# Kernel optimization log

Measured on AMD Instinct MI355X. Metric: run time of the kernel, lower is better.

The kernel has to match this reference:

```python
import jax, jax.numpy as jnp
import numpy as np

EMBED = 1024
B, I, J = 8, 2048, 2048
SCALE = EMBED ** -0.5


def setup_inputs() -> dict:
    key = jax.random.key(0)
    ks = jax.random.split(key, 5)
    s = EMBED ** -0.5  # init scale for weights
    return {
        "q_in": jax.random.normal(ks[0], (B, I, EMBED), dtype=jnp.float32),
        "k_v": jax.random.normal(ks[1], (B, J, EMBED), dtype=jnp.float32),
        "Wq": jax.random.normal(ks[2], (EMBED, EMBED), dtype=jnp.float32) * s,
        "bq": jnp.zeros((EMBED,), dtype=jnp.float32),
        "Wk": jax.random.normal(ks[3], (EMBED, EMBED), dtype=jnp.float32) * s,
        "bk": jnp.zeros((EMBED,), dtype=jnp.float32),
        "Wv": jax.random.normal(ks[4], (EMBED, EMBED), dtype=jnp.float32) * s,
        "bv": jnp.zeros((EMBED,), dtype=jnp.float32),
    }


def reference(q_in, k_v, Wq, bq, Wk, bk, Wv, bv):
    # Linear projections (torch Linear: x @ W.T + b; here W stored as [in, out])
    q = q_in @ Wq + bq            # [b, i, d]
    k = k_v @ Wk + bk             # [b, j, d]
    v = k_v @ Wv + bv             # [b, j, d]
    sim = jnp.einsum('bid,bjd->bij', q, k) * SCALE  # [b, i, j]
    attn = jax.nn.softmax(sim, axis=-1)
    # dropout with drop_rate=0.0 is identity
    out = jnp.einsum('bij,bjd->bid', attn, v)       # [b, i, d]
    return out
```

## Files before the change

kernel.cpp:

```cpp
#include <hip/hip_runtime.h>
#include <hip/hip_bf16.h>


#define BATCH 8
#define SEQ   2048
#define EMB   1024
#define SC2   0.045084222f

typedef __attribute__((ext_vector_type(8))) short bf16x8;
typedef __attribute__((ext_vector_type(4))) float f32x4;
typedef __attribute__((ext_vector_type(4))) unsigned short u16x4;
typedef __attribute__((ext_vector_type(8))) unsigned short u16x8;
typedef __attribute__((ext_vector_type(4))) unsigned int u32x4;
typedef __attribute__((ext_vector_type(4))) float fl4;

__device__ __forceinline__ unsigned short f2bf(float f) {
    unsigned u = __builtin_bit_cast(unsigned, f);
    unsigned r = u + 0x7fffu + ((u >> 16) & 1u);
    return (unsigned short)(r >> 16);
}
__device__ __forceinline__ float bf2f(unsigned short s) {
    return __builtin_bit_cast(float, ((unsigned)s) << 16);
}
__device__ __forceinline__ unsigned cvtpk(float a, float b) {
    unsigned r;
    asm("v_cvt_pk_bf16_f32 %0, %1, %2" : "=v"(r) : "v"(a), "v"(b));
    return r;
}
__device__ __forceinline__ void gload16(const unsigned short* g, unsigned short* l) {
    __builtin_amdgcn_global_load_lds(
        (const __attribute__((address_space(1))) void*)g,
        (__attribute__((address_space(3))) void*)l, 16, 0, 0);
}

__global__ __launch_bounds__(256)
void convert_w(const float* __restrict__ Wq, const float* __restrict__ Wk,
               const float* __restrict__ Wv, unsigned short* __restrict__ Wt)
{
    const int wsel = blockIdx.y;
    const float* W = (wsel == 0) ? Wq : (wsel == 1) ? Wk : Wv;
    unsigned short* O = Wt + (size_t)wsel * EMB * EMB;
    const int k0 = (blockIdx.x >> 4) * 64;
    const int n0 = (blockIdx.x & 15) * 64;
    __shared__ unsigned short l[64 * 65];
    const int tid = threadIdx.x;
#pragma unroll
    for (int it = 0; it < 16; it++) {
        const int lin = it * 256 + tid;
        const int k = lin >> 6, n = lin & 63;
        l[n * 65 + k] = f2bf(W[(size_t)(k0 + k) * EMB + n0 + n]);
    }
    __syncthreads();
#pragma unroll
    for (int it = 0; it < 16; it++) {
        const int lin = it * 256 + tid;
        const int n = lin >> 6, k = lin & 63;
        O[(size_t)(n0 + n) * EMB + k0 + k] = l[n * 65 + k];
    }
}

__device__ __forceinline__ void stageT(const unsigned short* lanebase, size_t rstride,
                                       unsigned short* lwave) {
#pragma unroll
    for (int i = 0; i < 2; i++)
        gload16(lanebase + (size_t)(i * 128) * rstride, lwave + i * 4096);
}

#define MFMA16_LO(A0,A1,A2,A3)                                                  \
        acc[0][0] = __builtin_amdgcn_mfma_f32_16x16x32_bf16(A0, bv0, acc[0][0], 0, 0, 0); \
        acc[0][1] = __builtin_amdgcn_mfma_f32_16x16x32_bf16(A0, bv1, acc[0][1], 0, 0, 0); \
        acc[0][2] = __builtin_amdgcn_mfma_f32_16x16x32_bf16(A0, bv2, acc[0][2], 0, 0, 0); \
        acc[0][3] = __builtin_amdgcn_mfma_f32_16x16x32_bf16(A0, bv3, acc[0][3], 0, 0, 0); \
        acc[1][0] = __builtin_amdgcn_mfma_f32_16x16x32_bf16(A1, bv0, acc[1][0], 0, 0, 0); \
        acc[1][1] = __builtin_amdgcn_mfma_f32_16x16x32_bf16(A1, bv1, acc[1][1], 0, 0, 0); \
        acc[1][2] = __builtin_amdgcn_mfma_f32_16x16x32_bf16(A1, bv2, acc[1][2], 0, 0, 0); \
        acc[1][3] = __builtin_amdgcn_mfma_f32_16x16x32_bf16(A1, bv3, acc[1][3], 0, 0, 0); \
        acc[2][0] = __builtin_amdgcn_mfma_f32_16x16x32_bf16(A2, bv0, acc[2][0], 0, 0, 0); \
        acc[2][1] = __builtin_amdgcn_mfma_f32_16x16x32_bf16(A2, bv1, acc[2][1], 0, 0, 0); \
        acc[2][2] = __builtin_amdgcn_mfma_f32_16x16x32_bf16(A2, bv2, acc[2][2], 0, 0, 0); \
        acc[2][3] = __builtin_amdgcn_mfma_f32_16x16x32_bf16(A2, bv3, acc[2][3], 0, 0, 0); \
        acc[3][0] = __builtin_amdgcn_mfma_f32_16x16x32_bf16(A3, bv0, acc[3][0], 0, 0, 0); \
        acc[3][1] = __builtin_amdgcn_mfma_f32_16x16x32_bf16(A3, bv1, acc[3][1], 0, 0, 0); \
        acc[3][2] = __builtin_amdgcn_mfma_f32_16x16x32_bf16(A3, bv2, acc[3][2], 0, 0, 0); \
        acc[3][3] = __builtin_amdgcn_mfma_f32_16x16x32_bf16(A3, bv3, acc[3][3], 0, 0, 0);

#define MFMA16_HI(A4,A5,A6,A7)                                                  \
        acc[4][0] = __builtin_amdgcn_mfma_f32_16x16x32_bf16(A4, bv0, acc[4][0], 0, 0, 0); \
        acc[4][1] = __builtin_amdgcn_mfma_f32_16x16x32_bf16(A4, bv1, acc[4][1], 0, 0, 0); \
        acc[4][2] = __builtin_amdgcn_mfma_f32_16x16x32_bf16(A4, bv2, acc[4][2], 0, 0, 0); \
        acc[4][3] = __builtin_amdgcn_mfma_f32_16x16x32_bf16(A4, bv3, acc[4][3], 0, 0, 0); \
        acc[5][0] = __builtin_amdgcn_mfma_f32_16x16x32_bf16(A5, bv0, acc[5][0], 0, 0, 0); \
        acc[5][1] = __builtin_amdgcn_mfma_f32_16x16x32_bf16(A5, bv1, acc[5][1], 0, 0, 0); \
        acc[5][2] = __builtin_amdgcn_mfma_f32_16x16x32_bf16(A5, bv2, acc[5][2], 0, 0, 0); \
        acc[5][3] = __builtin_amdgcn_mfma_f32_16x16x32_bf16(A5, bv3, acc[5][3], 0, 0, 0); \
        acc[6][0] = __builtin_amdgcn_mfma_f32_16x16x32_bf16(A6, bv0, acc[6][0], 0, 0, 0); \
        acc[6][1] = __builtin_amdgcn_mfma_f32_16x16x32_bf16(A6, bv1, acc[6][1], 0, 0, 0); \
        acc[6][2] = __builtin_amdgcn_mfma_f32_16x16x32_bf16(A6, bv2, acc[6][2], 0, 0, 0); \
        acc[6][3] = __builtin_amdgcn_mfma_f32_16x16x32_bf16(A6, bv3, acc[6][3], 0, 0, 0); \
        acc[7][0] = __builtin_amdgcn_mfma_f32_16x16x32_bf16(A7, bv0, acc[7][0], 0, 0, 0); \
        acc[7][1] = __builtin_amdgcn_mfma_f32_16x16x32_bf16(A7, bv1, acc[7][1], 0, 0, 0); \
        acc[7][2] = __builtin_amdgcn_mfma_f32_16x16x32_bf16(A7, bv2, acc[7][2], 0, 0, 0); \
        acc[7][3] = __builtin_amdgcn_mfma_f32_16x16x32_bf16(A7, bv3, acc[7][3], 0, 0, 0);

#define FRAG_READS(SLOT)                                                        \
        const unsigned short* pa = &sA[SLOT][0];                                \
        const unsigned short* pb = &sB[SLOT][0];                                \
        bf16x8 a0 = *(bf16x8*)&pa[aoff0];                                       \
        bf16x8 a1 = *(bf16x8*)&pa[aoff0 + 512];                                 \
        bf16x8 a2 = *(bf16x8*)&pa[aoff0 + 1024];                                \
        bf16x8 a3 = *(bf16x8*)&pa[aoff0 + 1536];                                \
        bf16x8 a4 = *(bf16x8*)&pa[aoff0 + 2048];                                \
        bf16x8 a5 = *(bf16x8*)&pa[aoff0 + 2560];                                \
        bf16x8 a6 = *(bf16x8*)&pa[aoff0 + 3072];                                \
        bf16x8 a7 = *(bf16x8*)&pa[aoff0 + 3584];                                \
        bf16x8 bv0 = *(bf16x8*)&pb[boff0];                                      \
        bf16x8 bv1 = *(bf16x8*)&pb[boff0 + 512];                                \
        bf16x8 bv2 = *(bf16x8*)&pb[boff0 + 1024];                               \
        bf16x8 bv3 = *(bf16x8*)&pb[boff0 + 1536];

__device__ __forceinline__ void pipe_gemm(
    const unsigned short* __restrict__ Asrc,
    const unsigned short* __restrict__ Bsrc,
    const size_t strideA, const size_t strideB, const int NT,
    unsigned short (*sA)[8192], unsigned short (*sB)[8192],
    const int lwave, const int aoff0, const int boff0,
    f32x4 acc[8][4])
{
    stageT(Asrc, strideA, &sA[0][lwave]);
    stageT(Bsrc, strideB, &sB[0][lwave]);
    stageT(Asrc + 32, strideA, &sA[1][lwave]);
    stageT(Bsrc + 32, strideB, &sB[1][lwave]);
    asm volatile("s_waitcnt vmcnt(4)" ::: "memory");
    __builtin_amdgcn_s_barrier();
    __builtin_amdgcn_sched_barrier(0);

    for (int T = 0; T < NT; ++T) {
        const int s = T & 3;
        const int doStage = (T + 2 < NT);
        const int s2 = (T + 2) & 3;
        {
            FRAG_READS(s)
            if (doStage) stageT(Asrc + (T + 2) * 32, strideA, &sA[s2][lwave]);
            __builtin_amdgcn_s_setprio(1);
            MFMA16_LO(a0, a1, a2, a3)
            __builtin_amdgcn_s_setprio(0);
            if (doStage) stageT(Bsrc + (T + 2) * 32, strideB, &sB[s2][lwave]);
            __builtin_amdgcn_s_setprio(1);
            MFMA16_HI(a4, a5, a6, a7)
            __builtin_amdgcn_s_setprio(0);
            if (doStage) { asm volatile("s_waitcnt vmcnt(4)" ::: "memory"); }
            else         { asm volatile("s_waitcnt vmcnt(0)" ::: "memory"); }
            __builtin_amdgcn_s_barrier();
            __builtin_amdgcn_sched_barrier(0);
        }
    }
}

#define ISSUEF(TT, R0, R1, R2, R3)                                              \
    {                                                                           \
        const float* fb_ = Fsrc + (size_t)(TT) * 32;                            \
        R0 = *(const fl4*)fb_;                                                  \
        R1 = *(const fl4*)(fb_ + 4);                                            \
        R2 = *(const fl4*)(fb_ + 128 * strideF);                                \
        R3 = *(const fl4*)(fb_ + 128 * strideF + 4);                            \
    }
#define WRITEF(SLOT, R0, R1, R2, R3)                                            \
    {                                                                           \
        unsigned short* d_ = &sF[SLOT][0] + tid * 8;                            \
        u32x4 w0, w1;                                                           \
        w0[0] = cvtpk(R0[0], R0[1]); w0[1] = cvtpk(R0[2], R0[3]);               \
        w0[2] = cvtpk(R1[0], R1[1]); w0[3] = cvtpk(R1[2], R1[3]);               \
        w1[0] = cvtpk(R2[0], R2[1]); w1[1] = cvtpk(R2[2], R2[3]);               \
        w1[2] = cvtpk(R3[0], R3[1]); w1[3] = cvtpk(R3[2], R3[3]);               \
        *(u32x4*)d_ = w0;                                                       \
        *(u32x4*)(d_ + 4096) = w1;                                              \
    }

template <bool F32A>
__device__ __forceinline__ void pipe_gemm_mx(
    const float* __restrict__ Fsrc,
    const unsigned short* __restrict__ Gsrc,
    const size_t strideF, const size_t strideG, const int NT,
    unsigned short (*sA)[8192], unsigned short (*sB)[8192],
    const int lwave, const int aoff0, const int boff0, const int tid,
    f32x4 acc[8][4])
{
    unsigned short (*sF)[8192] = F32A ? sA : sB;
    unsigned short (*sG)[8192] = F32A ? sB : sA;

    fl4 t0, t1, t2, t3, rf0, rf1, rf2, rf3;
    ISSUEF(0, t0, t1, t2, t3);
    ISSUEF(1, rf0, rf1, rf2, rf3);
    __builtin_amdgcn_sched_barrier(0);
    stageT(Gsrc,      strideG, &sG[0][lwave]);
    stageT(Gsrc + 32, strideG, &sG[1][lwave]);
    asm volatile("s_waitcnt vmcnt(2)" ::: "memory");
    WRITEF(0, t0, t1, t2, t3);
    asm volatile("s_waitcnt lgkmcnt(0)" ::: "memory");
    __builtin_amdgcn_s_barrier();
    __builtin_amdgcn_sched_barrier(0);

    for (int T = 0; T < NT; ++T) {
        const int s = T & 3;
        const int sw = (T + 1) & 3;
        const int s2 = (T + 2) & 3;
        const int wrPre = (T + 1 < NT);
        const int doLd  = (T + 2 < NT);
        {
            asm volatile("s_waitcnt vmcnt(2)" ::: "memory");
            if (wrPre) { WRITEF(sw, rf0, rf1, rf2, rf3); }
            if (doLd)  { ISSUEF(T + 2, rf0, rf1, rf2, rf3); }
            __builtin_amdgcn_sched_barrier(0);
            if (doLd)  stageT(Gsrc + (T + 2) * 32, strideG, &sG[s2][lwave]);
            FRAG_READS(s)
            __builtin_amdgcn_s_setprio(1);
            MFMA16_LO(a0, a1, a2, a3)
            __builtin_amdgcn_s_setprio(0);
            __builtin_amdgcn_s_setprio(1);
            MFMA16_HI(a4, a5, a6, a7)
            __builtin_amdgcn_s_setprio(0);
            if (doLd) { asm volatile("s_waitcnt vmcnt(6) lgkmcnt(0)" ::: "memory"); }
            else      { asm volatile("s_waitcnt vmcnt(0) lgkmcnt(0)" ::: "memory"); }
            __builtin_amdgcn_s_barrier();
            __builtin_amdgcn_sched_barrier(0);
        }
    }
}

#define PIPE_PREAMBLE                                                     \
    __shared__ unsigned short sMem[65536];                    \
    unsigned short (*sA)[8192] = (unsigned short (*)[8192])sMem;          \
    unsigned short (*sB)[8192] = (unsigned short (*)[8192])(sMem + 32768);\
    const int tid = threadIdx.x, lane = tid & 63;                         \
    const int wid = tid >> 6, wr = wid >> 2, wn = wid & 3;                \
    const int r = lane & 15, g = lane >> 4;                               \
    const int lwave = (wid << 9);                                         \
    const int scol = ((tid & 3) ^ ((tid >> 3) & 3)) * 8;                  \
    const int gsw = (g ^ ((r >> 1) & 3)) * 8;                             \
    const int aoff0 = (wr * 128 + r) * 32 + gsw;                          \
    const int boff0 = (wn * 64 + r) * 32 + gsw;                           \
    f32x4 acc[8][4];                                                      \
    _Pragma("unroll") for (int i_ = 0; i_ < 8; i_++)                      \
    _Pragma("unroll") for (int j_ = 0; j_ < 4; j_++) acc[i_][j_] = (f32x4)0.0f;

__device__ __forceinline__ void lds_flush_bf16(const unsigned short* sP,
                                               unsigned short* gbase,
                                               size_t gstride, int tid)
{
    const int lane = tid & 63, wv = tid >> 6;
    const int rowsel = lane >> 5, jj = lane & 31;
#pragma unroll
    for (int it = 0; it < 16; ++it) {
        const int row = it * 16 + wv * 2 + rowsel;
        const int byte = row * 512 + ((jj * 16) ^ ((row & 7) << 4));
        u16x8 v = *(const u16x8*)((const char*)sP + byte);
        *(u16x8*)&gbase[(size_t)row * gstride + jj * 8] = v;
    }
}

__global__ __launch_bounds__(512, 1)
void proj_all(const unsigned short* __restrict__ Wt,
              const float* __restrict__ q_in,
              const float* __restrict__ k_v,
              const float* __restrict__ bq, const float* __restrict__ bk,
              const float* __restrict__ bv,
              unsigned short* __restrict__ qb, unsigned short* __restrict__ kb,
              unsigned short* __restrict__ vt)
{
    PIPE_PREAMBLE
    const int bid = blockIdx.x;
    int d0 = 0, i0 = 0, m0 = 0, n0 = 0;
    const bool qrole = (bid < 256);
    if (qrole) {
        const int lid = (bid & 7) * 32 + (bid >> 3);
        d0 = (lid & 3) * 256; i0 = (lid >> 2) * 256;
        const unsigned short* Gsrc = Wt + (size_t)(d0 + (tid >> 2)) * EMB + scol;
        const float* Fsrc = q_in + (size_t)(i0 + (tid >> 2)) * EMB + scol;
        pipe_gemm_mx<false>(Fsrc, Gsrc, EMB, EMB, EMB / 32,
                            sA, sB, lwave, aoff0, boff0, tid, acc);
    } else {
        const int b2 = bid - 256;
        const int lid = (b2 & 7) * 64 + (b2 >> 3);
        n0 = (lid & 7) * 256; m0 = (lid >> 3) * 256;
        const float* Fsrc = k_v + (size_t)(m0 + (tid >> 2)) * EMB + scol;
        const unsigned short* Gsrc = Wt + (size_t)EMB * EMB
                                   + (size_t)(n0 + (tid >> 2)) * EMB + scol;
        pipe_gemm_mx<true>(Fsrc, Gsrc, EMB, EMB, EMB / 32,
                           sA, sB, lwave, aoff0, boff0, tid, acc);
    }

    if (qrole) {
#pragma unroll
        for (int mm = 0; mm < 8; mm++) {
            const int colb = wr * 128 + mm * 16 + g * 4;
            const fl4 b4 = *(const fl4*)&bq[d0 + colb];
#pragma unroll
            for (int n = 0; n < 4; n++) {
                const int row = wn * 64 + n * 16 + r;
                u16x4 u;
#pragma unroll
                for (int c = 0; c < 4; c++) u[c] = f2bf(acc[mm][n][c] + b4[c]);
                const int byte = row * 512 + ((colb * 2) ^ ((row & 7) << 4));
                *(u16x4*)((char*)sMem + byte) = u;
            }
        }
        __syncthreads();
        lds_flush_bf16(sMem, qb + (size_t)i0 * EMB + d0, EMB, tid);
    } else {
        const int b = m0 >> 11;
        const int j0l = m0 & 2047;
        if (n0 < 1024) {
#pragma unroll
            for (int mm = 0; mm < 8; mm++) {
                const int ibase = m0 + wr * 128 + mm * 16 + g * 4;
#pragma unroll
                for (int n = 0; n < 4; n++) {
                    const int col = n0 + wn * 64 + n * 16 + r;
                    const float bb = bk[col];
#pragma unroll
                    for (int c = 0; c < 4; c++)
                        kb[(size_t)(ibase + c) * EMB + col] = f2bf(acc[mm][n][c] + bb);
                }
            }
        } else {
#pragma unroll
            for (int mm = 0; mm < 8; mm++) {
                const int colb = wr * 128 + mm * 16 + g * 4;
#pragma unroll
                for (int n = 0; n < 4; n++) {
                    const int row = wn * 64 + n * 16 + r;
                    const float bb = bv[n0 - 1024 + row];
                    u16x4 u;
#pragma unroll
                    for (int c = 0; c < 4; c++) u[c] = f2bf(acc[mm][n][c] + bb);
                    const int byte = row * 512 + ((colb * 2) ^ ((row & 7) << 4));
                    *(u16x4*)((char*)sMem + byte) = u;
                }
            }
            __syncthreads();
            lds_flush_bf16(sMem, vt + ((size_t)b * EMB + (n0 - 1024)) * SEQ + j0l,
                           SEQ, tid);
        }
    }
}

__global__ __launch_bounds__(512, 1)
void qk256_kernel(const unsigned short* __restrict__ qb,
                  const unsigned short* __restrict__ kb,
                  unsigned short* __restrict__ P,
                  float* __restrict__ Ppart)
{
    PIPE_PREAMBLE
    const int bid = blockIdx.x;
    const int lid = (bid & 7) * 64 + (bid >> 3);
    const int b = lid >> 6, jt = (lid >> 3) & 7, it = lid & 7;
    const int j0 = jt * 256, i0 = it * 256;
    const unsigned short* Ag = kb + (size_t)b * SEQ * EMB;
    const unsigned short* Bg = qb + (size_t)b * SEQ * EMB;
    const unsigned short* Asrc = Ag + (size_t)(j0 + (tid >> 2)) * EMB + scol;
    const unsigned short* Bsrc = Bg + (size_t)(i0 + (tid >> 2)) * EMB + scol;

    pipe_gemm(Asrc, Bsrc, EMB, EMB, EMB / 32, sA, sB, lwave, aoff0, boff0, acc);

    float ps[4] = {0.f, 0.f, 0.f, 0.f};
#pragma unroll
    for (int mm = 0; mm < 8; mm++) {
        const int colb = wr * 128 + mm * 16 + g * 4;
#pragma unroll
        for (int n = 0; n < 4; n++) {
            const int row = wn * 64 + n * 16 + r;
            u16x4 u;
#pragma unroll
            for (int c = 0; c < 4; c++) {
                const float p = exp2f(acc[mm][n][c] * SC2);
                ps[n] += p;
                u[c] = f2bf(p);
            }
            const int byte = row * 512 + ((colb * 2) ^ ((row & 7) << 4));
            *(u16x4*)((char*)sMem + byte) = u;
        }
    }
#pragma unroll
    for (int n = 0; n < 4; n++) {
        ps[n] += __shfl_xor(ps[n], 16);
        ps[n] += __shfl_xor(ps[n], 32);
    }
    if (g == 0) {
        const int slot = jt * 2 + wr;
        float* pp = Ppart + (size_t)slot * (BATCH * SEQ) + (size_t)b * SEQ;
#pragma unroll
        for (int n = 0; n < 4; n++)
            pp[i0 + wn * 64 + n * 16 + r] = ps[n];
    }
    __syncthreads();
    unsigned short* Pb = P + (size_t)b * SEQ * SEQ;
    lds_flush_bf16(sMem, Pb + (size_t)i0 * SEQ + j0, SEQ, tid);
}

__global__ __launch_bounds__(512, 1)
void pv256_kernel(const unsigned short* __restrict__ P,
                  const unsigned short* __restrict__ vt,
                  const float* __restrict__ Ppart,
                  float* __restrict__ out)
{
    PIPE_PREAMBLE
    const int bid = blockIdx.x;
    const int lid = (bid & 7) * 32 + (bid >> 3);
    const int b = lid >> 5, it = (lid >> 2) & 7, dt = lid & 3;
    const int d0 = dt * 256, i0 = it * 256;
    const unsigned short* Ag = vt + (size_t)b * EMB * SEQ;
    const unsigned short* Bg = P + (size_t)b * SEQ * SEQ;
    const unsigned short* Asrc = Ag + (size_t)(d0 + (tid >> 2)) * SEQ + scol;
    const unsigned short* Bsrc = Bg + (size_t)(i0 + (tid >> 2)) * SEQ + scol;

    float inv[4];
#pragma unroll
    for (int n = 0; n < 4; n++) {
        const int row = b * SEQ + i0 + wn * 64 + n * 16 + r;
        float s = 0.f;
#pragma unroll
        for (int slot = 0; slot < 16; slot++)
            s += Ppart[(size_t)slot * (BATCH * SEQ) + row];
        inv[n] = 1.0f / s;
    }

    pipe_gemm(Asrc, Bsrc, SEQ, SEQ, SEQ / 32, sA, sB, lwave, aoff0, boff0, acc);

    float* ob = out + (size_t)b * SEQ * EMB;
    float* sF = (float*)sMem;
#pragma unroll
    for (int h = 0; h < 2; h++) {
        if (wr == h) {
#pragma unroll
            for (int mm = 0; mm < 8; mm++) {
                const int colb = mm * 16 + g * 4;
#pragma unroll
                for (int n = 0; n < 4; n++) {
                    const int row = wn * 64 + n * 16 + r;
                    fl4 o;
#pragma unroll
                    for (int c = 0; c < 4; c++) o[c] = acc[mm][n][c] * inv[n];
                    const int byte = row * 512 + ((colb * 4) ^ ((row & 7) << 4));
                    *(fl4*)((char*)sF + byte) = o;
                }
            }
        }
        __syncthreads();
        {
            const int rowsel = lane >> 5, jj = lane & 31;
#pragma unroll
            for (int itx = 0; itx < 16; ++itx) {
                const int row = itx * 16 + wid * 2 + rowsel;
                const int byte = row * 512 + ((jj * 16) ^ ((row & 7) << 4));
                fl4 v = *(const fl4*)((const char*)sF + byte);
                *(fl4*)&ob[(size_t)(i0 + row) * EMB + d0 + h * 128 + jj * 4] = v;
            }
        }
        if (h == 0) __syncthreads();
    }
}

extern "C" void kernel_launch(void* const* d_in, const int* in_sizes, int n_in,
                              void* d_out, int out_size, void* d_ws, size_t ws_size,
                              hipStream_t stream)
{
    const float* q_in = (const float*)d_in[0];
    const float* k_v  = (const float*)d_in[1];
    const float* Wq   = (const float*)d_in[2];
    const float* bq   = (const float*)d_in[3];
    const float* Wk   = (const float*)d_in[4];
    const float* bk   = (const float*)d_in[5];
    const float* Wv   = (const float*)d_in[6];
    const float* bv   = (const float*)d_in[7];
    float* out = (float*)d_out;

    char* ws = (char*)d_ws;
    unsigned short* P    = (unsigned short*)(ws);
    unsigned short* qb   = (unsigned short*)(ws + (size_t)67108864);
    unsigned short* kb   = (unsigned short*)(ws + (size_t)100663296);
    unsigned short* vt   = (unsigned short*)(ws + (size_t)134217728);
    unsigned short* Wt   = (unsigned short*)(ws + (size_t)167772160);
    float*          Ppart= (float*)(ws + (size_t)174063616);

    convert_w<<<dim3(256, 3), 256, 0, stream>>>(Wq, Wk, Wv, Wt);
    proj_all<<<768, 512, 0, stream>>>(Wt, q_in, k_v, bq, bk, bv, qb, kb, vt);
    qk256_kernel<<<512, 512, 0, stream>>>(qb, kb, P, Ppart);
    pv256_kernel<<<256, 512, 0, stream>>>(P, vt, Ppart, out);
}
```

Measured before the change: 292.6 us.

## Double-buffer fp32 prefetch registers and defer LDS write past MFMAs in mixed GEMM

The mixed fp32/bf16 GEMM pipeline now alternates two register sets for the fp32 operand, unrolled by two tiles. The next tile's global load is issued into a free set, and the previous set is converted and written to LDS after the MFMAs, not before. The goal is to stop the conversion and LDS store from sitting on the critical path and to hide global load latency behind compute. In exchange it uses more registers and the loop now assumes an even tile count.

```diff
diff --git a/kernel.cpp b/kernel.cpp
--- a/kernel.cpp
+++ b/kernel.cpp
@@ -176,6 +176,28 @@
         *(u32x4*)(d_ + 4096) = w1;                                              \
     }
 
+#define PIPE_TILE_MX(T, I0,I1,I2,I3, W0,W1,W2,W3)                               \
+    {                                                                           \
+        const int s_ = (T) & 3, sw_ = ((T) + 1) & 3, s2_ = ((T) + 2) & 3;       \
+        const int doLd_ = ((T) + 2 < NT), doWr_ = ((T) + 1 < NT);               \
+        if (doLd_) { ISSUEF((T) + 2, I0, I1, I2, I3); }                         \
+        __builtin_amdgcn_sched_barrier(0);                                      \
+        if (doLd_) stageT(Gsrc + ((T) + 2) * 32, strideG, &sG[s2_][lwave]);     \
+        FRAG_READS(s_)                                                          \
+        __builtin_amdgcn_s_setprio(1);                                          \
+        MFMA16_LO(a0, a1, a2, a3)                                               \
+        __builtin_amdgcn_s_setprio(0);                                          \
+        __builtin_amdgcn_s_setprio(1);                                          \
+        MFMA16_HI(a4, a5, a6, a7)                                               \
+        __builtin_amdgcn_s_setprio(0);                                          \
+        if (doWr_) { WRITEF(sw_, W0, W1, W2, W3); }                             \
+        if (doLd_) { asm volatile("s_waitcnt vmcnt(6)" ::: "memory"); }         \
+        else       { asm volatile("s_waitcnt vmcnt(0)" ::: "memory"); }         \
+        asm volatile("s_waitcnt lgkmcnt(0)" ::: "memory");                      \
+        __builtin_amdgcn_s_barrier();                                           \
+        __builtin_amdgcn_sched_barrier(0);                                      \
+    }
+
 template <bool F32A>
 __device__ __forceinline__ void pipe_gemm_mx(
     const float* __restrict__ Fsrc,
@@ -188,42 +210,21 @@
     unsigned short (*sF)[8192] = F32A ? sA : sB;
     unsigned short (*sG)[8192] = F32A ? sB : sA;
 
-    fl4 t0, t1, t2, t3, rf0, rf1, rf2, rf3;
-    ISSUEF(0, t0, t1, t2, t3);
-    ISSUEF(1, rf0, rf1, rf2, rf3);
+    fl4 p0, p1, p2, p3, q0, q1, q2, q3;
+    ISSUEF(0, p0, p1, p2, p3);
+    ISSUEF(1, q0, q1, q2, q3);
     __builtin_amdgcn_sched_barrier(0);
     stageT(Gsrc,      strideG, &sG[0][lwave]);
     stageT(Gsrc + 32, strideG, &sG[1][lwave]);
+    WRITEF(0, p0, p1, p2, p3);
     asm volatile("s_waitcnt vmcnt(2)" ::: "memory");
-    WRITEF(0, t0, t1, t2, t3);
     asm volatile("s_waitcnt lgkmcnt(0)" ::: "memory");
     __builtin_amdgcn_s_barrier();
     __builtin_amdgcn_sched_barrier(0);
 
-    for (int T = 0; T < NT; ++T) {
-        const int s = T & 3;
-        const int sw = (T + 1) & 3;
-        const int s2 = (T + 2) & 3;
-        const int wrPre = (T + 1 < NT);
-        const int doLd  = (T + 2 < NT);
-        {
-            asm volatile("s_waitcnt vmcnt(2)" ::: "memory");
-            if (wrPre) { WRITEF(sw, rf0, rf1, rf2, rf3); }
-            if (doLd)  { ISSUEF(T + 2, rf0, rf1, rf2, rf3); }
-            __builtin_amdgcn_sched_barrier(0);
-            if (doLd)  stageT(Gsrc + (T + 2) * 32, strideG, &sG[s2][lwave]);
-            FRAG_READS(s)
-            __builtin_amdgcn_s_setprio(1);
-            MFMA16_LO(a0, a1, a2, a3)
-            __builtin_amdgcn_s_setprio(0);
-            __builtin_amdgcn_s_setprio(1);
-            MFMA16_HI(a4, a5, a6, a7)
-            __builtin_amdgcn_s_setprio(0);
-            if (doLd) { asm volatile("s_waitcnt vmcnt(6) lgkmcnt(0)" ::: "memory"); }
-            else      { asm volatile("s_waitcnt vmcnt(0) lgkmcnt(0)" ::: "memory"); }
-            __builtin_amdgcn_s_barrier();
-            __builtin_amdgcn_sched_barrier(0);
-        }
+    for (int T = 0; T < NT; T += 2) {
+        PIPE_TILE_MX(T,     p0, p1, p2, p3, q0, q1, q2, q3);
+        PIPE_TILE_MX(T + 1, q0, q1, q2, q3, p0, p1, p2, p3);
     }
 }
 
@@ -427,6 +428,7 @@
     pipe_gemm(Asrc, Bsrc, SEQ, SEQ, SEQ / 32, sA, sB, lwave, aoff0, boff0, acc);
 
     float* ob = out + (size_t)b * SEQ * EMB;
+    const float* rsb = nullptr; (void)rsb;
     float* sF = (float*)sMem;
 #pragma unroll
     for (int h = 0; h < 2; h++) {
```

After: 311.7 us. +6.5%, slower.
